# Kernel tuning notes

Measured on AMD Instinct MI355X. Metric: run time of the kernel, lower is better.

## Reference

```python
import jax, jax.numpy as jnp
import numpy as np
import math

B, H, S, D = 2, 16, 2048, 128

def setup_inputs() -> dict:
    key = jax.random.key(0)
    kq, kk, kv = jax.random.split(key, 3)
    return {
        "query": jax.random.normal(kq, (B, H, S, D), dtype=jnp.float32),
        "key": jax.random.normal(kk, (B, H, S, D), dtype=jnp.float32),
        "value": jax.random.normal(kv, (B, H, S, D), dtype=jnp.float32),
        "m": 0,  # falsy mask: original's masked_fill was non-in-place (no-op) anyway
    }

def reference(query, key, value, m):
    d = query.shape[-1]
    # scores: [B, H, S, S]
    scores = jnp.einsum("bhqd,bhkd->bhqk", query, key) / math.sqrt(d)
    # NOTE: original torch code's masked_fill is not in-place, so the mask
    # never affects scores; we faithfully skip it (m is falsy here regardless).
    p_attn = jax.nn.softmax(scores, axis=-1)
    p_val = jnp.einsum("bhqk,bhkd->bhqd", p_attn, value)
    return (p_val, p_attn)
```

## Files before the change

kernel.cpp:

```cpp
#include <hip/hip_runtime.h>
#include <hip/hip_bf16.h>
#include <math.h>

#define S_LEN 2048
#define DHEAD 128
#define NH    32
#define BM    128
#define KT    32
#define NKT   (S_LEN / KT)
#define VROW  40
#define SCALE 0.08838834764831845f
#define CMAX  16.0f

typedef __attribute__((ext_vector_type(4))) float f32x4;
typedef __attribute__((ext_vector_type(8))) _Float16 f16x8;
typedef __attribute__((ext_vector_type(4))) unsigned short u16x4;
typedef __attribute__((ext_vector_type(8))) unsigned short u16x8;

static __device__ __forceinline__ f16x8 as_h8(u16x8 x) {
  return __builtin_bit_cast(f16x8, x);
}
static __device__ __forceinline__ unsigned short h16(float x) {
  _Float16 h = (_Float16)x;
  return __builtin_bit_cast(unsigned short, h);
}

#define BAR()                                                   \
  do {                                                          \
    __builtin_amdgcn_sched_barrier(0);                          \
    asm volatile("s_waitcnt lgkmcnt(0)" ::: "memory");          \
    __builtin_amdgcn_s_barrier();                               \
    __builtin_amdgcn_sched_barrier(0);                          \
  } while (0)

__global__ __launch_bounds__(512, 4) void attn_kernel(
    const float* __restrict__ Qg, const float* __restrict__ Kg,
    const float* __restrict__ Vg, float* __restrict__ out) {
  __shared__ __align__(16) unsigned short khf[2][KT * DHEAD];
  __shared__ __align__(16) unsigned short vtr[2][DHEAD * VROW];

  const int tid = threadIdx.x;
  const int w  = tid >> 6;
  const int l  = tid & 63;
  const int lr = l & 15;
  const int lg = l >> 4;

  const int d_  = blockIdx.x;
  const int xcd = d_ & 7;
  const int slot = d_ >> 3;
  const int bh = xcd + 8 * (slot >> 4);
  const int qb = slot & 15;

  const size_t head_off = (size_t)bh * S_LEN * DHEAD;
  const float* Qh = Qg + head_off;
  const float* Kh = Kg + head_off;
  const float* Vh = Vg + head_off;
  float* Ov = out + head_off;
  float* Pa = out + (size_t)NH * S_LEN * DHEAD + (size_t)bh * S_LEN * S_LEN;

  const int kkv0 = tid >> 5, kd4 = tid & 31;
  const int kkv1 = kkv0 + 16;
  const int kaddr0 = kkv0 * 128 + (((kd4 >> 1) ^ (kkv0 & 7)) << 3) + ((kd4 & 1) << 2);
  const int kaddr1 = kkv1 * 128 + (((kd4 >> 1) ^ (kkv1 & 7)) << 3) + ((kd4 & 1) << 2);
  float4 kx0, kx1;
  auto load_k = [&](int t) {
    const float4* s = (const float4*)(Kh + (size_t)t * KT * DHEAD);
    kx0 = s[tid];
    kx1 = s[512 + tid];
  };
  auto write_k = [&](int b) {
    u16x4 a, c;
    a[0] = h16(kx0.x); a[1] = h16(kx0.y); a[2] = h16(kx0.z); a[3] = h16(kx0.w);
    c[0] = h16(kx1.x); c[1] = h16(kx1.y); c[2] = h16(kx1.z); c[3] = h16(kx1.w);
    *(u16x4*)&khf[b][kaddr0] = a;
    *(u16x4*)&khf[b][kaddr1] = c;
  };
  auto ldk = [&](int b, int row, int kc) -> f16x8 {
    return as_h8(*(const u16x8*)&khf[b][row * 128 +
                                        (((kc * 4 + lg) ^ (row & 7)) << 3)]);
  };

  const int vd = w * 16 + lr;
  const int mg = lg;
  float vv0, vv1, vv2, vv3, vv4, vv5, vv6, vv7;
  auto load_v = [&](int t) {
    const float* s = Vh + (size_t)t * KT * DHEAD + vd;
    vv0 = s[(2 * mg) * 128];      vv1 = s[(2 * mg + 16) * 128];
    vv2 = s[(2 * mg + 1) * 128];  vv3 = s[(2 * mg + 17) * 128];
    vv4 = s[(2 * mg + 8) * 128];  vv5 = s[(2 * mg + 24) * 128];
    vv6 = s[(2 * mg + 9) * 128];  vv7 = s[(2 * mg + 25) * 128];
  };
  auto write_v = [&](int b) {
    u16x4 a, c;
    a[0] = h16(vv0); a[1] = h16(vv1); a[2] = h16(vv2); a[3] = h16(vv3);
    c[0] = h16(vv4); c[1] = h16(vv5); c[2] = h16(vv6); c[3] = h16(vv7);
    *(u16x4*)&vtr[b][vd * VROW + mg * 4] = a;
    *(u16x4*)&vtr[b][vd * VROW + (mg + 4) * 4] = c;
  };

  load_k(0);
  const int qrow = qb * BM + w * 16 + lr;
  const float* qptr = Qh + (size_t)qrow * DHEAD;
  f16x8 qh[4];
#pragma unroll
  for (int kc = 0; kc < 4; ++kc) {
    const float4* qp4 = (const float4*)(qptr + kc * 32 + lg * 8);
    float4 a = qp4[0], b = qp4[1];
    float xs[8] = {a.x, a.y, a.z, a.w, b.x, b.y, b.z, b.w};
#pragma unroll
    for (int i = 0; i < 8; ++i) qh[kc][i] = (_Float16)(xs[i] * SCALE);
  }

  const f32x4 zero4 = {0.f, 0.f, 0.f, 0.f};

  float esum = 0.f;
  for (int t = 0; t < NKT; ++t) {
    const int b = t & 1;
    write_k(b);
    BAR();
    if (t + 1 < NKT) {
      load_k(t + 1);
    } else {
      load_k(0);
      load_v(0);
    }

    f32x4 sacc0 = zero4, sacc1 = zero4;
    __builtin_amdgcn_s_setprio(1);
#pragma unroll
    for (int kc = 0; kc < 4; ++kc) {
      sacc0 = __builtin_amdgcn_mfma_f32_16x16x32_f16(ldk(b, lr, kc), qh[kc],
                                                     sacc0, 0, 0, 0);
      sacc1 = __builtin_amdgcn_mfma_f32_16x16x32_f16(ldk(b, lr + 16, kc), qh[kc],
                                                     sacc1, 0, 0, 0);
    }
    __builtin_amdgcn_s_setprio(0);
#pragma unroll
    for (int r = 0; r < 4; ++r)
      esum += __expf(sacc0[r] - CMAX) + __expf(sacc1[r] - CMAX);
  }
  esum += __shfl_xor(esum, 16);
  esum += __shfl_xor(esum, 32);
  const float off_ = CMAX + logf(esum);

  f32x4 oacc[8];
#pragma unroll
  for (int dt = 0; dt < 8; ++dt) oacc[dt] = zero4;

  float* Prow = Pa + (size_t)(qb * BM + w * 16 + lr) * S_LEN;

  for (int t = 0; t < NKT; ++t) {
    const int b = t & 1;
    write_k(b);
    write_v(b);
    BAR();
    if (t + 1 < NKT) {
      load_k(t + 1);
      load_v(t + 1);
    }

    f32x4 sacc0 = zero4, sacc1 = zero4;
    __builtin_amdgcn_s_setprio(1);
#pragma unroll
    for (int kc = 0; kc < 4; ++kc) {
      sacc0 = __builtin_amdgcn_mfma_f32_16x16x32_f16(ldk(b, lr, kc), qh[kc],
                                                     sacc0, 0, 0, 0);
      sacc1 = __builtin_amdgcn_mfma_f32_16x16x32_f16(ldk(b, lr + 16, kc), qh[kc],
                                                     sacc1, 0, 0, 0);
    }
    __builtin_amdgcn_s_setprio(0);

    f32x4 pv0, pv1;
#pragma unroll
    for (int r = 0; r < 4; ++r) {
      pv0[r] = __expf(sacc0[r] - off_);
      pv1[r] = __expf(sacc1[r] - off_);
    }
    *(f32x4*)&Prow[t * KT + lg * 4] = pv0;
    *(f32x4*)&Prow[t * KT + 16 + lg * 4] = pv1;

    f16x8 pa;
    {
      auto p0 = __builtin_amdgcn_cvt_pkrtz(pv0[0], pv1[0]);
      auto p1 = __builtin_amdgcn_cvt_pkrtz(pv0[1], pv1[1]);
      auto p2 = __builtin_amdgcn_cvt_pkrtz(pv0[2], pv1[2]);
      auto p3 = __builtin_amdgcn_cvt_pkrtz(pv0[3], pv1[3]);
      pa[0] = p0[0]; pa[1] = p0[1]; pa[2] = p1[0]; pa[3] = p1[1];
      pa[4] = p2[0]; pa[5] = p2[1]; pa[6] = p3[0]; pa[7] = p3[1];
    }

    __builtin_amdgcn_s_setprio(1);
    const unsigned short* vsrc = vtr[b];
#pragma unroll
    for (int dt = 0; dt < 8; ++dt) {
      u16x8 vf = *(const u16x8*)&vsrc[(dt * 16 + lr) * VROW + lg * 8];
      oacc[dt] = __builtin_amdgcn_mfma_f32_16x16x32_f16(pa, as_h8(vf),
                                                        oacc[dt], 0, 0, 0);
    }
    __builtin_amdgcn_s_setprio(0);
  }

#pragma unroll
  for (int dt = 0; dt < 8; ++dt) {
#pragma unroll
    for (int r = 0; r < 4; ++r) {
      const int qloc = w * 16 + lg * 4 + r;
      Ov[(size_t)(qb * BM + qloc) * DHEAD + dt * 16 + lr] = oacc[dt][r];
    }
  }
}

extern "C" void kernel_launch(void* const* d_in, const int* in_sizes, int n_in,
                              void* d_out, int out_size, void* d_ws,
                              size_t ws_size, hipStream_t stream) {
  const float* Q = (const float*)d_in[0];
  const float* K = (const float*)d_in[1];
  const float* V = (const float*)d_in[2];
  float* out = (float*)d_out;
  (void)in_sizes; (void)n_in; (void)out_size; (void)d_ws; (void)ws_size;
  dim3 grid(NH * (S_LEN / BM));
  attn_kernel<<<grid, 512, 0, stream>>>(Q, K, V, out);
}
```

Measured before the change: 302.5 us.

## Split tile loop into barrier-separated phases interleaving loads with MFMA clusters

Each K/V tile iteration is restructured into several phases separated by workgroup barriers. Each phase issues LDS fragment reads and a slice of the next tile's global loads, waits on LDS, then runs a short MFMA cluster at raised priority. This ping-pong style schedule is meant to overlap memory traffic with matrix work across waves, and it adds many extra s_barrier instructions per tile, which could cost synchronization overhead.

Result: slower. 361.1 us (+19.4%).

```diff
diff --git a/kernel.cpp b/kernel.cpp
--- a/kernel.cpp
+++ b/kernel.cpp
@@ -25,11 +25,24 @@
   return __builtin_bit_cast(unsigned short, h);
 }
 
+#define MFMA16(a, b, c) __builtin_amdgcn_mfma_f32_16x16x32_f16(a, b, c, 0, 0, 0)
+
 #define BAR()                                                   \
   do {                                                          \
     __builtin_amdgcn_sched_barrier(0);                          \
     asm volatile("s_waitcnt lgkmcnt(0)" ::: "memory");          \
     __builtin_amdgcn_s_barrier();                               \
+    __builtin_amdgcn_sched_barrier(0);                          \
+  } while (0)
+#define PH_BAR()                                                \
+  do {                                                          \
+    __builtin_amdgcn_sched_barrier(0);                          \
+    __builtin_amdgcn_s_barrier();                               \
+    __builtin_amdgcn_sched_barrier(0);                          \
+  } while (0)
+#define LGKM0()                                                 \
+  do {                                                          \
+    asm volatile("s_waitcnt lgkmcnt(0)" ::: "memory");          \
     __builtin_amdgcn_sched_barrier(0);                          \
   } while (0)
 
@@ -63,11 +76,6 @@
   const int kaddr0 = kkv0 * 128 + (((kd4 >> 1) ^ (kkv0 & 7)) << 3) + ((kd4 & 1) << 2);
   const int kaddr1 = kkv1 * 128 + (((kd4 >> 1) ^ (kkv1 & 7)) << 3) + ((kd4 & 1) << 2);
   float4 kx0, kx1;
-  auto load_k = [&](int t) {
-    const float4* s = (const float4*)(Kh + (size_t)t * KT * DHEAD);
-    kx0 = s[tid];
-    kx1 = s[512 + tid];
-  };
   auto write_k = [&](int b) {
     u16x4 a, c;
     a[0] = h16(kx0.x); a[1] = h16(kx0.y); a[2] = h16(kx0.z); a[3] = h16(kx0.w);
@@ -98,7 +106,11 @@
     *(u16x4*)&vtr[b][vd * VROW + (mg + 4) * 4] = c;
   };
 
-  load_k(0);
+  {
+    const float4* s = (const float4*)Kh;
+    kx0 = s[tid];
+    kx1 = s[512 + tid];
+  }
   const int qrow = qb * BM + w * 16 + lr;
   const float* qptr = Qh + (size_t)qrow * DHEAD;
   f16x8 qh[4];
@@ -118,23 +130,35 @@
     const int b = t & 1;
     write_k(b);
     BAR();
-    if (t + 1 < NKT) {
-      load_k(t + 1);
-    } else {
-      load_k(0);
-      load_v(0);
-    }
-
     f32x4 sacc0 = zero4, sacc1 = zero4;
-    __builtin_amdgcn_s_setprio(1);
-#pragma unroll
-    for (int kc = 0; kc < 4; ++kc) {
-      sacc0 = __builtin_amdgcn_mfma_f32_16x16x32_f16(ldk(b, lr, kc), qh[kc],
-                                                     sacc0, 0, 0, 0);
-      sacc1 = __builtin_amdgcn_mfma_f32_16x16x32_f16(ldk(b, lr + 16, kc), qh[kc],
-                                                     sacc1, 0, 0, 0);
-    }
-    __builtin_amdgcn_s_setprio(0);
+    {
+      f16x8 ka0 = ldk(b, lr, 0), kb0 = ldk(b, lr + 16, 0);
+      f16x8 ka1 = ldk(b, lr, 1), kb1 = ldk(b, lr + 16, 1);
+      if (t + 1 < NKT) kx0 = ((const float4*)(Kh + (size_t)(t + 1) * KT * DHEAD))[tid];
+      PH_BAR(); LGKM0();
+      __builtin_amdgcn_s_setprio(1);
+      sacc0 = MFMA16(ka0, qh[0], sacc0); sacc1 = MFMA16(kb0, qh[0], sacc1);
+      sacc0 = MFMA16(ka1, qh[1], sacc0); sacc1 = MFMA16(kb1, qh[1], sacc1);
+      __builtin_amdgcn_s_setprio(0);
+      PH_BAR();
+    }
+    {
+      f16x8 ka2 = ldk(b, lr, 2), kb2 = ldk(b, lr + 16, 2);
+      f16x8 ka3 = ldk(b, lr, 3), kb3 = ldk(b, lr + 16, 3);
+      if (t + 1 < NKT) {
+        kx1 = ((const float4*)(Kh + (size_t)(t + 1) * KT * DHEAD))[512 + tid];
+      } else {
+        const float4* s = (const float4*)Kh;
+        kx0 = s[tid];
+        kx1 = s[512 + tid];
+        load_v(0);
+      }
+      PH_BAR(); LGKM0();
+      __builtin_amdgcn_s_setprio(1);
+      sacc0 = MFMA16(ka2, qh[2], sacc0); sacc1 = MFMA16(kb2, qh[2], sacc1);
+      sacc0 = MFMA16(ka3, qh[3], sacc0); sacc1 = MFMA16(kb3, qh[3], sacc1);
+      __builtin_amdgcn_s_setprio(0);
+    }
 #pragma unroll
     for (int r = 0; r < 4; ++r)
       esum += __expf(sacc0[r] - CMAX) + __expf(sacc1[r] - CMAX);
@@ -154,50 +178,72 @@
     write_k(b);
     write_v(b);
     BAR();
-    if (t + 1 < NKT) {
-      load_k(t + 1);
-      load_v(t + 1);
-    }
-
     f32x4 sacc0 = zero4, sacc1 = zero4;
-    __builtin_amdgcn_s_setprio(1);
-#pragma unroll
-    for (int kc = 0; kc < 4; ++kc) {
-      sacc0 = __builtin_amdgcn_mfma_f32_16x16x32_f16(ldk(b, lr, kc), qh[kc],
-                                                     sacc0, 0, 0, 0);
-      sacc1 = __builtin_amdgcn_mfma_f32_16x16x32_f16(ldk(b, lr + 16, kc), qh[kc],
-                                                     sacc1, 0, 0, 0);
-    }
-    __builtin_amdgcn_s_setprio(0);
-
-    f32x4 pv0, pv1;
-#pragma unroll
-    for (int r = 0; r < 4; ++r) {
-      pv0[r] = __expf(sacc0[r] - off_);
-      pv1[r] = __expf(sacc1[r] - off_);
-    }
-    *(f32x4*)&Prow[t * KT + lg * 4] = pv0;
-    *(f32x4*)&Prow[t * KT + 16 + lg * 4] = pv1;
-
-    f16x8 pa;
-    {
-      auto p0 = __builtin_amdgcn_cvt_pkrtz(pv0[0], pv1[0]);
-      auto p1 = __builtin_amdgcn_cvt_pkrtz(pv0[1], pv1[1]);
-      auto p2 = __builtin_amdgcn_cvt_pkrtz(pv0[2], pv1[2]);
-      auto p3 = __builtin_amdgcn_cvt_pkrtz(pv0[3], pv1[3]);
-      pa[0] = p0[0]; pa[1] = p0[1]; pa[2] = p1[0]; pa[3] = p1[1];
-      pa[4] = p2[0]; pa[5] = p2[1]; pa[6] = p3[0]; pa[7] = p3[1];
-    }
-
-    __builtin_amdgcn_s_setprio(1);
-    const unsigned short* vsrc = vtr[b];
-#pragma unroll
-    for (int dt = 0; dt < 8; ++dt) {
-      u16x8 vf = *(const u16x8*)&vsrc[(dt * 16 + lr) * VROW + lg * 8];
-      oacc[dt] = __builtin_amdgcn_mfma_f32_16x16x32_f16(pa, as_h8(vf),
-                                                        oacc[dt], 0, 0, 0);
-    }
-    __builtin_amdgcn_s_setprio(0);
+    {
+      f16x8 ka0 = ldk(b, lr, 0), kb0 = ldk(b, lr + 16, 0);
+      f16x8 ka1 = ldk(b, lr, 1), kb1 = ldk(b, lr + 16, 1);
+      if (t + 1 < NKT) kx0 = ((const float4*)(Kh + (size_t)(t + 1) * KT * DHEAD))[tid];
+      PH_BAR(); LGKM0();
+      __builtin_amdgcn_s_setprio(1);
+      sacc0 = MFMA16(ka0, qh[0], sacc0); sacc1 = MFMA16(kb0, qh[0], sacc1);
+      sacc0 = MFMA16(ka1, qh[1], sacc0); sacc1 = MFMA16(kb1, qh[1], sacc1);
+      __builtin_amdgcn_s_setprio(0);
+      PH_BAR();
+    }
+    {
+      f16x8 ka2 = ldk(b, lr, 2), kb2 = ldk(b, lr + 16, 2);
+      f16x8 ka3 = ldk(b, lr, 3), kb3 = ldk(b, lr + 16, 3);
+      if (t + 1 < NKT) kx1 = ((const float4*)(Kh + (size_t)(t + 1) * KT * DHEAD))[512 + tid];
+      PH_BAR(); LGKM0();
+      __builtin_amdgcn_s_setprio(1);
+      sacc0 = MFMA16(ka2, qh[2], sacc0); sacc1 = MFMA16(kb2, qh[2], sacc1);
+      sacc0 = MFMA16(ka3, qh[3], sacc0); sacc1 = MFMA16(kb3, qh[3], sacc1);
+      __builtin_amdgcn_s_setprio(0);
+      PH_BAR();
+    }
+    {
+      u16x8 vf0 = *(const u16x8*)&vtr[b][(0 * 16 + lr) * VROW + lg * 8];
+      u16x8 vf1 = *(const u16x8*)&vtr[b][(1 * 16 + lr) * VROW + lg * 8];
+      u16x8 vf2 = *(const u16x8*)&vtr[b][(2 * 16 + lr) * VROW + lg * 8];
+      u16x8 vf3 = *(const u16x8*)&vtr[b][(3 * 16 + lr) * VROW + lg * 8];
+      if (t + 1 < NKT) load_v(t + 1);
+      f32x4 pv0, pv1;
+#pragma unroll
+      for (int r = 0; r < 4; ++r) {
+        pv0[r] = __expf(sacc0[r] - off_);
+        pv1[r] = __expf(sacc1[r] - off_);
+      }
+      *(f32x4*)&Prow[t * KT + lg * 4] = pv0;
+      *(f32x4*)&Prow[t * KT + 16 + lg * 4] = pv1;
+      f16x8 pa;
+      {
+        auto p0 = __builtin_amdgcn_cvt_pkrtz(pv0[0], pv1[0]);
+        auto p1 = __builtin_amdgcn_cvt_pkrtz(pv0[1], pv1[1]);
+        auto p2 = __builtin_amdgcn_cvt_pkrtz(pv0[2], pv1[2]);
+        auto p3 = __builtin_amdgcn_cvt_pkrtz(pv0[3], pv1[3]);
+        pa[0] = p0[0]; pa[1] = p0[1]; pa[2] = p1[0]; pa[3] = p1[1];
+        pa[4] = p2[0]; pa[5] = p2[1]; pa[6] = p3[0]; pa[7] = p3[1];
+      }
+      PH_BAR(); LGKM0();
+      __builtin_amdgcn_s_setprio(1);
+      oacc[0] = MFMA16(pa, as_h8(vf0), oacc[0]);
+      oacc[1] = MFMA16(pa, as_h8(vf1), oacc[1]);
+      oacc[2] = MFMA16(pa, as_h8(vf2), oacc[2]);
+      oacc[3] = MFMA16(pa, as_h8(vf3), oacc[3]);
+      __builtin_amdgcn_s_setprio(0);
+      PH_BAR();
+      u16x8 vf4 = *(const u16x8*)&vtr[b][(4 * 16 + lr) * VROW + lg * 8];
+      u16x8 vf5 = *(const u16x8*)&vtr[b][(5 * 16 + lr) * VROW + lg * 8];
+      u16x8 vf6 = *(const u16x8*)&vtr[b][(6 * 16 + lr) * VROW + lg * 8];
+      u16x8 vf7 = *(const u16x8*)&vtr[b][(7 * 16 + lr) * VROW + lg * 8];
+      PH_BAR(); LGKM0();
+      __builtin_amdgcn_s_setprio(1);
+      oacc[4] = MFMA16(pa, as_h8(vf4), oacc[4]);
+      oacc[5] = MFMA16(pa, as_h8(vf5), oacc[5]);
+      oacc[6] = MFMA16(pa, as_h8(vf6), oacc[6]);
+      oacc[7] = MFMA16(pa, as_h8(vf7), oacc[7]);
+      __builtin_amdgcn_s_setprio(0);
+    }
   }
 
 #pragma unroll
```
